# Kernel optimization log

Measured on AMD Instinct MI355X. Metric: run time of the kernel, lower is better.

## Reference

```python
import jax, jax.numpy as jnp
import numpy as np
from jax import lax

B, H, W_IN, C = 32, 32, 32, 128   # NHWC input
KH, KW = 3, 3                     # kernel size (padding 'same', stride 1)
F = 512                           # filters


def setup_inputs() -> dict:
    key = jax.random.key(0)
    ks = jax.random.split(key, 10)
    # sparse factor shapes: (KH*KW*C, 1152), (1152, F), (F, F)
    d0, d1, d2, d3 = KH * KW * C, 1152, F, F
    x = jax.random.normal(ks[0], (B, H, W_IN, C), dtype=jnp.float32)
    k0 = jax.random.normal(ks[1], (d0, d1), dtype=jnp.float32) * (1.0 / np.sqrt(d0))
    k1 = jax.random.normal(ks[2], (d1, d2), dtype=jnp.float32) * (1.0 / np.sqrt(d1))
    k2 = jax.random.normal(ks[3], (d2, d3), dtype=jnp.float32) * (1.0 / np.sqrt(d2))
    # fixed binary sparsity masks (K.constant in the original build)
    m0 = jax.random.bernoulli(ks[4], 0.1, (d0, d1)).astype(jnp.float32)
    m1 = jax.random.bernoulli(ks[5], 0.1, (d1, d2)).astype(jnp.float32)
    m2 = jax.random.bernoulli(ks[6], 0.1, (d2, d3)).astype(jnp.float32)
    scale = jax.random.normal(ks[7], (1,), dtype=jnp.float32)
    bias = jax.random.normal(ks[8], (F,), dtype=jnp.float32) * 0.01
    return {"x": x, "k0": k0, "k1": k1, "k2": k2,
            "m0": m0, "m1": m1, "m2": m2, "scale": scale, "bias": bias}


def reference(x, k0, k1, k2, m0, m1, m2, scale, bias):
    # Chained masked sparse factors collapse (associativity) to one effective
    # filter matrix of shape (KH*KW*C, F); the im2col row flatten order in the
    # original is (h, w, c), which matches an HWIO reshape exactly.
    w_eff = (k0 * m0) @ (k1 * m1) @ (k2 * m2)          # (KH*KW*C, F)
    w = (w_eff * scale[0]).reshape(KH, KW, C, F)        # fold scalar scale into kernel
    out = lax.conv_general_dilated(
        x, w, window_strides=(1, 1), padding='SAME',
        dimension_numbers=('NHWC', 'HWIO', 'NHWC'))     # (B, H, W, F)
    return out + bias
```

## Files before the change

### kernel.cpp

```cpp
#include <hip/hip_runtime.h>

typedef __attribute__((ext_vector_type(8))) short short8;
typedef __attribute__((ext_vector_type(4))) float f32x4;

typedef __attribute__((address_space(1))) const unsigned gas_u32;
typedef __attribute__((address_space(3))) unsigned las_u32;

static __device__ __forceinline__ void g2l16(const void* g, void* l) {
  __builtin_amdgcn_global_load_lds((gas_u32*)g, (las_u32*)l, 16, 0, 0);
}

static __device__ __forceinline__ short f2bf(float f) {
  union { float f; unsigned u; } v; v.f = f;
  unsigned r = (v.u + 0x7FFFu + ((v.u >> 16) & 1u)) >> 16;
  return (short)r;
}

#define MF(a_, b_, c_) __builtin_amdgcn_mfma_f32_16x16x32_bf16(a_, b_, c_, 0, 0, 0)

static __device__ __forceinline__ void xcvt_body(const float* __restrict__ x,
                                                 short* __restrict__ xbp, int i) {
  int c8 = i & 15;
  int t = i >> 4;
  int wp = t % 34, t2 = t / 34;
  int hp = t2 % 34, b = t2 / 34;
  short8 o = {};
  if (hp >= 1 && hp <= 32 && wp >= 1 && wp <= 32) {
    const f32x4* s = (const f32x4*)(x + (((size_t)((b << 5) + hp - 1) << 5) + (wp - 1)) * 128 + c8 * 8);
    f32x4 a = s[0], bb2 = s[1];
    o[0] = f2bf(a[0]); o[1] = f2bf(a[1]); o[2] = f2bf(a[2]); o[3] = f2bf(a[3]);
    o[4] = f2bf(bb2[0]); o[5] = f2bf(bb2[1]); o[6] = f2bf(bb2[2]); o[7] = f2bf(bb2[3]);
  }
  ((short8*)xbp)[i] = o;
}

__global__ __launch_bounds__(256) void k_prepw(const float* __restrict__ k0f,
                                               const float* __restrict__ m0f,
                                               const float* __restrict__ scf,
                                               const float* __restrict__ k1f,
                                               const float* __restrict__ m1f,
                                               const float* __restrict__ k2f,
                                               const float* __restrict__ m2f,
                                               short* __restrict__ w1b,
                                               short* __restrict__ w2T,
                                               short* __restrict__ w3T,
                                               const float* __restrict__ x,
                                               short* __restrict__ xbp) {
  __shared__ float tile[32][33];
  const int bb = blockIdx.x, tid = threadIdx.x;
  if (bb < 648) {
    int i = bb * 256 + tid;
    float s = scf[0];
    const f32x4* kk = (const f32x4*)k0f + (size_t)i * 2;
    const f32x4* mm = (const f32x4*)m0f + (size_t)i * 2;
    f32x4 a0 = kk[0], a1 = kk[1], b0 = mm[0], b1 = mm[1];
    short8 o;
    o[0] = f2bf(a0[0] * b0[0] * s); o[1] = f2bf(a0[1] * b0[1] * s);
    o[2] = f2bf(a0[2] * b0[2] * s); o[3] = f2bf(a0[3] * b0[3] * s);
    o[4] = f2bf(a1[0] * b1[0] * s); o[5] = f2bf(a1[1] * b1[1] * s);
    o[6] = f2bf(a1[2] * b1[2] * s); o[7] = f2bf(a1[3] * b1[3] * s);
    ((short8*)w1b)[i] = o;
  } else if (bb < 1480) {
    const float *kf, *mf; short* outp; int D, F, idx;
    if (bb < 1224) { kf = k1f; mf = m1f; outp = w2T; D = 1152; F = 512; idx = bb - 648; }
    else           { kf = k2f; mf = m2f; outp = w3T; D = 512;  F = 512; idx = bb - 1224; }
    int f0 = (idx & 15) * 32, d0 = (idx >> 4) * 32;
    int tx = tid & 31, ty = tid >> 5;
#pragma unroll
    for (int i = 0; i < 4; ++i) {
      int d = d0 + ty + i * 8;
      size_t ix = (size_t)d * F + f0 + tx;
      tile[ty + i * 8][tx] = kf[ix] * mf[ix];
    }
    __syncthreads();
#pragma unroll
    for (int i = 0; i < 4; ++i) {
      int f = f0 + ty + i * 8;
      outp[(size_t)f * D + d0 + tx] = f2bf(tile[tx][ty + i * 8]);
    }
  } else {
    xcvt_body(x, xbp, (bb - 1480) * 256 + tid);
  }
}

__global__ __launch_bounds__(256) void k_gemmx(const short* __restrict__ A,
                                               const short* __restrict__ BT,
                                               short* __restrict__ C, int M, int N, int K,
                                               const float* __restrict__ x,
                                               short* __restrict__ xbp, int xoff) {
  __shared__ __align__(16) short As[2][64][128];
  __shared__ __align__(16) short Bs[2][64][128];
  if (blockIdx.x >= 144) {
    xcvt_body(x, xbp, (xoff + (int)blockIdx.x - 144) * 256 + (int)threadIdx.x);
    return;
  }
  const int ntiles = N >> 6;
  const int m0 = (blockIdx.x / ntiles) << 6, n0 = (blockIdx.x % ntiles) << 6;
  const int tid = threadIdx.x;
  const int lane = tid & 63, wv = tid >> 6;
  const int wr = (wv >> 1) * 32, wc = (wv & 1) * 32;
  const int lr = lane & 15, lh = lane >> 4;

  const int rr = tid >> 4, sl = tid & 15;
  const int swz = sl ^ (rr & 7);
  const unsigned aOff = (unsigned)(m0 + rr) * K + swz * 8;
  const unsigned bOff = (unsigned)(n0 + rr) * K + swz * 8;
  const int ldsRow = 4 * wv;

  f32x4 acc[2][2] = {};

#define GST(buf_, kt_) do { \
    _Pragma("unroll") for (int j = 0; j < 4; ++j) \
      g2l16(A + aOff + (unsigned)j * 16u * (unsigned)K + (unsigned)(kt_) * 128u, \
            &As[buf_][j * 16 + ldsRow][0]); \
    _Pragma("unroll") for (int j = 0; j < 4; ++j) \
      g2l16(BT + bOff + (unsigned)j * 16u * (unsigned)K + (unsigned)(kt_) * 128u, \
            &Bs[buf_][j * 16 + ldsRow][0]); \
  } while (0)

  const int nk = K >> 7;
  GST(0, 0);
  asm volatile("s_waitcnt vmcnt(0)" ::: "memory");
  __builtin_amdgcn_s_barrier();

  for (int kt = 0; kt < nk; ++kt) {
    const int cur = kt & 1;
    if (kt + 1 < nk) { if (cur) GST(0, kt + 1); else GST(1, kt + 1); }
#pragma unroll
    for (int ks = 0; ks < 4; ++ks) {
      short8 af[2], bf[2];
#pragma unroll
      for (int i = 0; i < 2; ++i)
        af[i] = *(const short8*)&As[cur][wr + i * 16 + lr][((ks * 4 + lh) ^ (lr & 7)) * 8];
#pragma unroll
      for (int i = 0; i < 2; ++i)
        bf[i] = *(const short8*)&Bs[cur][wc + i * 16 + lr][((ks * 4 + lh) ^ (lr & 7)) * 8];
#pragma unroll
      for (int mi = 0; mi < 2; ++mi)
#pragma unroll
        for (int ni = 0; ni < 2; ++ni)
          acc[mi][ni] = MF(af[mi], bf[ni], acc[mi][ni]);
    }
    if (kt + 1 < nk) asm volatile("s_waitcnt vmcnt(0)" ::: "memory");
    __builtin_amdgcn_s_barrier();
  }
#pragma unroll
  for (int mi = 0; mi < 2; ++mi) {
    const int row = m0 + wr + mi * 16 + lh * 4;
#pragma unroll
    for (int ni = 0; ni < 2; ++ni) {
      const int col = n0 + wc + ni * 16 + lr;
#pragma unroll
      for (int q = 0; q < 4; ++q)
        C[(size_t)(row + q) * N + col] = f2bf(acc[mi][ni][q]);
    }
  }
#undef GST
}

#define RD_A(mf_, ks_) \
  (*(const short8*)&As[wr * 128 + (mf_) * 16 + lr][(((ks_) * 4 + lh) ^ (lr & 7)) * 8])
#define RD_B(nf_, ks_) \
  (*(const short8*)&Bs[wc * 64 + (nf_) * 16 + lr][(((ks_) * 4 + lh) ^ (lr & 7)) * 8])

#define LOADB do { \
  bfr[0][0] = RD_B(0, 0); bfr[0][1] = RD_B(0, 1); \
  bfr[1][0] = RD_B(1, 0); bfr[1][1] = RD_B(1, 1); \
  bfr[2][0] = RD_B(2, 0); bfr[2][1] = RD_B(2, 1); \
  bfr[3][0] = RD_B(3, 0); bfr[3][1] = RD_B(3, 1); } while (0)

#define STAGE_AQ(q_, tt_) do { \
  const int tc_ = (tt_) > 17 ? 17 : (tt_); \
  const int khw_ = tc_ >> 1; const int kh_ = (khw_ * 11) >> 5; const int kw_ = khw_ - kh_ * 3; \
  const int ao_ = (kh_ * 34 + kw_) * 128 + ((tc_ & 1) << 6) + (q_) * 4352; \
  g2l16(xbp + aBase + ao_, &As[(q_) * 32 + ldsA][0]); \
  g2l16(xbp + aBase + 17408 + ao_, &As[128 + (q_) * 32 + ldsA][0]); } while (0)

#define STAGE_B(tt_) do { \
  const int tc_ = (tt_) > 17 ? 17 : (tt_); \
  g2l16(wT + bBase +     tc_ * 64, &Bs[     ldsA][0]); \
  g2l16(wT + bBase + 36864 + tc_ * 64, &Bs[32 + ldsA][0]); \
  g2l16(wT + bBase + 73728 + tc_ * 64, &Bs[64 + ldsA][0]); \
  g2l16(wT + bBase + 110592 + tc_ * 64, &Bs[96 + ldsA][0]); } while (0)

#define MFMA16(p_) \
  acc[2*(p_)  ][0] = MF(a0k0, bfr[0][0], acc[2*(p_)  ][0]); \
  acc[2*(p_)  ][1] = MF(a0k0, bfr[1][0], acc[2*(p_)  ][1]); \
  acc[2*(p_)  ][2] = MF(a0k0, bfr[2][0], acc[2*(p_)  ][2]); \
  acc[2*(p_)  ][3] = MF(a0k0, bfr[3][0], acc[2*(p_)  ][3]); \
  acc[2*(p_)+1][0] = MF(a1k0, bfr[0][0], acc[2*(p_)+1][0]); \
  acc[2*(p_)+1][1] = MF(a1k0, bfr[1][0], acc[2*(p_)+1][1]); \
  acc[2*(p_)+1][2] = MF(a1k0, bfr[2][0], acc[2*(p_)+1][2]); \
  acc[2*(p_)+1][3] = MF(a1k0, bfr[3][0], acc[2*(p_)+1][3]); \
  acc[2*(p_)  ][0] = MF(a0k1, bfr[0][1], acc[2*(p_)  ][0]); \
  acc[2*(p_)  ][1] = MF(a0k1, bfr[1][1], acc[2*(p_)  ][1]); \
  acc[2*(p_)  ][2] = MF(a0k1, bfr[2][1], acc[2*(p_)  ][2]); \
  acc[2*(p_)  ][3] = MF(a0k1, bfr[3][1], acc[2*(p_)  ][3]); \
  acc[2*(p_)+1][0] = MF(a1k1, bfr[0][1], acc[2*(p_)+1][0]); \
  acc[2*(p_)+1][1] = MF(a1k1, bfr[1][1], acc[2*(p_)+1][1]); \
  acc[2*(p_)+1][2] = MF(a1k1, bfr[2][1], acc[2*(p_)+1][2]); \
  acc[2*(p_)+1][3] = MF(a1k1, bfr[3][1], acc[2*(p_)+1][3]);

#define PHASE(p_, PRE, WAITV, ...) do { \
  PRE; \
  short8 a0k0 = RD_A(2*(p_), 0),   a0k1 = RD_A(2*(p_), 1); \
  short8 a1k0 = RD_A(2*(p_)+1, 0), a1k1 = RD_A(2*(p_)+1, 1); \
  __VA_ARGS__ \
  asm volatile("s_waitcnt lgkmcnt(0)" ::: "memory"); \
  __builtin_amdgcn_sched_barrier(0); \
  __builtin_amdgcn_s_setprio(1); \
  MFMA16(p_) \
  __builtin_amdgcn_s_setprio(0); \
  WAITV; \
  __builtin_amdgcn_s_barrier(); \
} while (0)

#define VM4 asm volatile("s_waitcnt vmcnt(4)" ::: "memory")
#define VM6 asm volatile("s_waitcnt vmcnt(6)" ::: "memory")
#define VM8 asm volatile("s_waitcnt vmcnt(8)" ::: "memory")

__global__ __launch_bounds__(256, 2) void k_conv(const short* __restrict__ xbp,
                                                 const short* __restrict__ wT,
                                                 const float* __restrict__ bias,
                                                 float* __restrict__ out) {
  __shared__ __align__(16) short As[256][64];
  __shared__ __align__(16) short Bs[128][64];
  int bid = blockIdx.x;
  bid = (bid & 7) * 64 + (bid >> 3);
  const int mt = bid >> 2, nt = bid & 3;
  const int m0 = mt << 8, n0 = nt << 7;
  const int tid = threadIdx.x;
  const int lane = tid & 63, wid = tid >> 6;
  const int wr = wid >> 1, wc = wid & 1;
  const int lr = lane & 15, lh = lane >> 4;

  f32x4 acc[8][4] = {};
  short8 bfr[4][2];

  const int rsub = tid >> 3;
  const int sw = (tid & 7) ^ (rsub & 7);
  const int ldsA = wid * 8;

  const int Mb = m0 + rsub;
  const int b = Mb >> 10, h0 = (Mb >> 5) & 31, w = Mb & 31;
  const unsigned aBase = (unsigned)((b * 34 + h0) * 34 + w) * 128 + sw * 8;
  const unsigned bBase = (unsigned)(n0 + rsub) * 1152 + sw * 8;

  STAGE_B(0);
  STAGE_AQ(0, 0); STAGE_AQ(1, 0); STAGE_AQ(2, 0);
  asm volatile("s_waitcnt vmcnt(0)" ::: "memory");
  __builtin_amdgcn_s_barrier();

  for (int t = 0; t < 18; ++t) {
    const int tn = t + 1;
    PHASE(0, LOADB, VM4, STAGE_AQ(3, t););
    PHASE(1, ,      VM6, STAGE_B(tn););
    PHASE(2, ,      VM8, STAGE_AQ(0, tn); STAGE_AQ(1, tn););
    PHASE(3, ,      VM4, STAGE_AQ(2, tn););
  }
  asm volatile("s_waitcnt vmcnt(0)" ::: "memory");

  const int orow = m0 + wr * 128, ocol = n0 + wc * 64;
#pragma unroll
  for (int mf = 0; mf < 8; ++mf) {
    const int row = orow + mf * 16 + lh * 4;
#pragma unroll
    for (int nf = 0; nf < 4; ++nf) {
      const int col = ocol + nf * 16 + lr;
      const float bv = bias[col];
#pragma unroll
      for (int q = 0; q < 4; ++q)
        out[(size_t)(row + q) * 512 + col] = acc[mf][nf][q] + bv;
    }
  }
}

extern "C" void kernel_launch(void* const* d_in, const int* in_sizes, int n_in,
                              void* d_out, int out_size, void* d_ws, size_t ws_size,
                              hipStream_t stream) {
  (void)in_sizes; (void)n_in; (void)out_size; (void)ws_size;
  const float* x    = (const float*)d_in[0];
  const float* k0   = (const float*)d_in[1];
  const float* k1   = (const float*)d_in[2];
  const float* k2   = (const float*)d_in[3];
  const float* m0   = (const float*)d_in[4];
  const float* m1   = (const float*)d_in[5];
  const float* m2   = (const float*)d_in[6];
  const float* sc   = (const float*)d_in[7];
  const float* bias = (const float*)d_in[8];
  float* out = (float*)d_out;
  char* ws = (char*)d_ws;

  short* xbp = (short*)(ws);
  short* w1b = (short*)(ws + 9469952);
  short* w2T = (short*)(ws + 12124160);
  short* w3T = (short*)(ws + 13303808);
  short* A1b = (short*)(ws + 13828096);
  short* wET = (short*)(ws + 15007744);

  k_prepw<<<2248, 256, 0, stream>>>(k0, m0, sc, k1, m1, k2, m2, w1b, w2T, w3T, x, xbp);
  k_gemmx<<<916, 256, 0, stream>>>(w1b, w2T, A1b, 1152, 512, 1152, x, xbp, 768);
  k_gemmx<<<916, 256, 0, stream>>>(w3T, A1b, wET, 512, 1152, 512, x, xbp, 1540);
  k_conv<<<512, 256, 0, stream>>>(xbp, wET, bias, out);
}
```

Baseline: 69.28 us.

## Double-buffer A fragments in registers to overlap LDS reads with MFMA

Restructures the per-phase loop so the A fragments for the next phase are read from LDS into a second register set while the current phase's MFMAs run. The explicit lgkmcnt(0) wait before each MFMA block is removed, and the global-to-LDS staging order and vmcnt waits are rearranged so all four A quarters are prefetched up front. The aim is to hide LDS read latency behind matrix math. It costs extra VGPRs for the second fragment set, and correctness depends on the compiler inserting the right LDS waits, which could alter the LDS data hazards between stage and read.

New measurement: 68.94 us. About the same (-0.5%).

```diff
diff --git a/kernel.cpp b/kernel.cpp
--- a/kernel.cpp
+++ b/kernel.cpp
@@ -163,12 +163,6 @@
 #define RD_B(nf_, ks_) \
   (*(const short8*)&Bs[wc * 64 + (nf_) * 16 + lr][(((ks_) * 4 + lh) ^ (lr & 7)) * 8])
 
-#define LOADB do { \
-  bfr[0][0] = RD_B(0, 0); bfr[0][1] = RD_B(0, 1); \
-  bfr[1][0] = RD_B(1, 0); bfr[1][1] = RD_B(1, 1); \
-  bfr[2][0] = RD_B(2, 0); bfr[2][1] = RD_B(2, 1); \
-  bfr[3][0] = RD_B(3, 0); bfr[3][1] = RD_B(3, 1); } while (0)
-
 #define STAGE_AQ(q_, tt_) do { \
   const int tc_ = (tt_) > 17 ? 17 : (tt_); \
   const int khw_ = tc_ >> 1; const int kh_ = (khw_ * 11) >> 5; const int kw_ = khw_ - kh_ * 3; \
@@ -178,46 +172,33 @@
 
 #define STAGE_B(tt_) do { \
   const int tc_ = (tt_) > 17 ? 17 : (tt_); \
-  g2l16(wT + bBase +     tc_ * 64, &Bs[     ldsA][0]); \
-  g2l16(wT + bBase + 36864 + tc_ * 64, &Bs[32 + ldsA][0]); \
-  g2l16(wT + bBase + 73728 + tc_ * 64, &Bs[64 + ldsA][0]); \
+  g2l16(wT + bBase +          tc_ * 64, &Bs[     ldsA][0]); \
+  g2l16(wT + bBase +  36864 + tc_ * 64, &Bs[32 + ldsA][0]); \
+  g2l16(wT + bBase +  73728 + tc_ * 64, &Bs[64 + ldsA][0]); \
   g2l16(wT + bBase + 110592 + tc_ * 64, &Bs[96 + ldsA][0]); } while (0)
 
-#define MFMA16(p_) \
-  acc[2*(p_)  ][0] = MF(a0k0, bfr[0][0], acc[2*(p_)  ][0]); \
-  acc[2*(p_)  ][1] = MF(a0k0, bfr[1][0], acc[2*(p_)  ][1]); \
-  acc[2*(p_)  ][2] = MF(a0k0, bfr[2][0], acc[2*(p_)  ][2]); \
-  acc[2*(p_)  ][3] = MF(a0k0, bfr[3][0], acc[2*(p_)  ][3]); \
-  acc[2*(p_)+1][0] = MF(a1k0, bfr[0][0], acc[2*(p_)+1][0]); \
-  acc[2*(p_)+1][1] = MF(a1k0, bfr[1][0], acc[2*(p_)+1][1]); \
-  acc[2*(p_)+1][2] = MF(a1k0, bfr[2][0], acc[2*(p_)+1][2]); \
-  acc[2*(p_)+1][3] = MF(a1k0, bfr[3][0], acc[2*(p_)+1][3]); \
-  acc[2*(p_)  ][0] = MF(a0k1, bfr[0][1], acc[2*(p_)  ][0]); \
-  acc[2*(p_)  ][1] = MF(a0k1, bfr[1][1], acc[2*(p_)  ][1]); \
-  acc[2*(p_)  ][2] = MF(a0k1, bfr[2][1], acc[2*(p_)  ][2]); \
-  acc[2*(p_)  ][3] = MF(a0k1, bfr[3][1], acc[2*(p_)  ][3]); \
-  acc[2*(p_)+1][0] = MF(a1k1, bfr[0][1], acc[2*(p_)+1][0]); \
-  acc[2*(p_)+1][1] = MF(a1k1, bfr[1][1], acc[2*(p_)+1][1]); \
-  acc[2*(p_)+1][2] = MF(a1k1, bfr[2][1], acc[2*(p_)+1][2]); \
-  acc[2*(p_)+1][3] = MF(a1k1, bfr[3][1], acc[2*(p_)+1][3]);
-
-#define PHASE(p_, PRE, WAITV, ...) do { \
-  PRE; \
-  short8 a0k0 = RD_A(2*(p_), 0),   a0k1 = RD_A(2*(p_), 1); \
-  short8 a1k0 = RD_A(2*(p_)+1, 0), a1k1 = RD_A(2*(p_)+1, 1); \
-  __VA_ARGS__ \
-  asm volatile("s_waitcnt lgkmcnt(0)" ::: "memory"); \
-  __builtin_amdgcn_sched_barrier(0); \
-  __builtin_amdgcn_s_setprio(1); \
-  MFMA16(p_) \
-  __builtin_amdgcn_s_setprio(0); \
-  WAITV; \
-  __builtin_amdgcn_s_barrier(); \
-} while (0)
+#define MFMA_PH(p_, x0_, x1_, x2_, x3_) \
+  acc[2*(p_)  ][0] = MF(x0_, bfr[0][0], acc[2*(p_)  ][0]); \
+  acc[2*(p_)  ][1] = MF(x0_, bfr[1][0], acc[2*(p_)  ][1]); \
+  acc[2*(p_)  ][2] = MF(x0_, bfr[2][0], acc[2*(p_)  ][2]); \
+  acc[2*(p_)  ][3] = MF(x0_, bfr[3][0], acc[2*(p_)  ][3]); \
+  acc[2*(p_)+1][0] = MF(x2_, bfr[0][0], acc[2*(p_)+1][0]); \
+  acc[2*(p_)+1][1] = MF(x2_, bfr[1][0], acc[2*(p_)+1][1]); \
+  acc[2*(p_)+1][2] = MF(x2_, bfr[2][0], acc[2*(p_)+1][2]); \
+  acc[2*(p_)+1][3] = MF(x2_, bfr[3][0], acc[2*(p_)+1][3]); \
+  acc[2*(p_)  ][0] = MF(x1_, bfr[0][1], acc[2*(p_)  ][0]); \
+  acc[2*(p_)  ][1] = MF(x1_, bfr[1][1], acc[2*(p_)  ][1]); \
+  acc[2*(p_)  ][2] = MF(x1_, bfr[2][1], acc[2*(p_)  ][2]); \
+  acc[2*(p_)  ][3] = MF(x1_, bfr[3][1], acc[2*(p_)  ][3]); \
+  acc[2*(p_)+1][0] = MF(x3_, bfr[0][1], acc[2*(p_)+1][0]); \
+  acc[2*(p_)+1][1] = MF(x3_, bfr[1][1], acc[2*(p_)+1][1]); \
+  acc[2*(p_)+1][2] = MF(x3_, bfr[2][1], acc[2*(p_)+1][2]); \
+  acc[2*(p_)+1][3] = MF(x3_, bfr[3][1], acc[2*(p_)+1][3]);
 
 #define VM4 asm volatile("s_waitcnt vmcnt(4)" ::: "memory")
-#define VM6 asm volatile("s_waitcnt vmcnt(6)" ::: "memory")
 #define VM8 asm volatile("s_waitcnt vmcnt(8)" ::: "memory")
+#define SBAR __builtin_amdgcn_s_barrier()
+#define SCHED0 __builtin_amdgcn_sched_barrier(0)
 
 __global__ __launch_bounds__(256, 2) void k_conv(const short* __restrict__ xbp,
                                                  const short* __restrict__ wT,
@@ -236,6 +217,7 @@
 
   f32x4 acc[8][4] = {};
   short8 bfr[4][2];
+  short8 aA0, aA1, aA2, aA3, aB0, aB1, aB2, aB3;
 
   const int rsub = tid >> 3;
   const int sw = (tid & 7) ^ (rsub & 7);
@@ -247,16 +229,51 @@
   const unsigned bBase = (unsigned)(n0 + rsub) * 1152 + sw * 8;
 
   STAGE_B(0);
-  STAGE_AQ(0, 0); STAGE_AQ(1, 0); STAGE_AQ(2, 0);
+  STAGE_AQ(0, 0); STAGE_AQ(1, 0); STAGE_AQ(2, 0); STAGE_AQ(3, 0);
   asm volatile("s_waitcnt vmcnt(0)" ::: "memory");
-  __builtin_amdgcn_s_barrier();
+  SBAR;
+  aA0 = RD_A(0, 0); aA1 = RD_A(0, 1); aA2 = RD_A(1, 0); aA3 = RD_A(1, 1);
 
   for (int t = 0; t < 18; ++t) {
     const int tn = t + 1;
-    PHASE(0, LOADB, VM4, STAGE_AQ(3, t););
-    PHASE(1, ,      VM6, STAGE_B(tn););
-    PHASE(2, ,      VM8, STAGE_AQ(0, tn); STAGE_AQ(1, tn););
-    PHASE(3, ,      VM4, STAGE_AQ(2, tn););
+    {
+      bfr[0][0] = RD_B(0, 0); bfr[1][0] = RD_B(1, 0); bfr[2][0] = RD_B(2, 0); bfr[3][0] = RD_B(3, 0);
+      bfr[0][1] = RD_B(0, 1); bfr[1][1] = RD_B(1, 1); bfr[2][1] = RD_B(2, 1); bfr[3][1] = RD_B(3, 1);
+      aB0 = RD_A(2, 0); aB1 = RD_A(2, 1); aB2 = RD_A(3, 0); aB3 = RD_A(3, 1);
+      STAGE_AQ(0, tn);
+      SCHED0;
+      __builtin_amdgcn_s_setprio(1);
+      MFMA_PH(0, aA0, aA1, aA2, aA3)
+      __builtin_amdgcn_s_setprio(0);
+      VM4; SBAR;
+    }
+    {
+      aA0 = RD_A(4, 0); aA1 = RD_A(4, 1); aA2 = RD_A(5, 0); aA3 = RD_A(5, 1);
+      STAGE_B(tn); STAGE_AQ(1, tn);
+      SCHED0;
+      __builtin_amdgcn_s_setprio(1);
+      MFMA_PH(1, aB0, aB1, aB2, aB3)
+      __builtin_amdgcn_s_setprio(0);
+      VM8; SBAR;
+    }
+    {
+      aB0 = RD_A(6, 0); aB1 = RD_A(6, 1); aB2 = RD_A(7, 0); aB3 = RD_A(7, 1);
+      STAGE_AQ(2, tn);
+      SCHED0;
+      __builtin_amdgcn_s_setprio(1);
+      MFMA_PH(2, aA0, aA1, aA2, aA3)
+      __builtin_amdgcn_s_setprio(0);
+      VM8; SBAR;
+    }
+    {
+      aA0 = RD_A(0, 0); aA1 = RD_A(0, 1); aA2 = RD_A(1, 0); aA3 = RD_A(1, 1);
+      STAGE_AQ(3, tn);
+      SCHED0;
+      __builtin_amdgcn_s_setprio(1);
+      MFMA_PH(3, aB0, aB1, aB2, aB3)
+      __builtin_amdgcn_s_setprio(0);
+      VM4; SBAR;
+    }
   }
   asm volatile("s_waitcnt vmcnt(0)" ::: "memory");
 
```

## Load A fragments directly from global into registers, double-buffer B in LDS

Applied to the files above, without the earlier changes.

Drops the LDS staging of the activation tile (A) and has each lane load its MFMA A-fragments straight from the padded bf16 input in global memory. The weight tile (B) becomes double-buffered in LDS, with one barrier per K-step instead of four phase barriers. The aim is to free LDS, cut barrier and LDS traffic and the instruction overhead of the phased schedule. In exchange, each lane issues uncoalesced-ish 16-byte global loads whose latency sits directly before the MFMAs. A rows are duplicated across the two column waves, which doubles global/L2 reads.

New measurement: 105.9 us. 1.53x slower.

```diff
diff --git a/kernel.cpp b/kernel.cpp
--- a/kernel.cpp
+++ b/kernel.cpp
@@ -158,73 +158,21 @@
 #undef GST
 }
 
-#define RD_A(mf_, ks_) \
-  (*(const short8*)&As[wr * 128 + (mf_) * 16 + lr][(((ks_) * 4 + lh) ^ (lr & 7)) * 8])
-#define RD_B(nf_, ks_) \
-  (*(const short8*)&Bs[wc * 64 + (nf_) * 16 + lr][(((ks_) * 4 + lh) ^ (lr & 7)) * 8])
-
-#define LOADB do { \
-  bfr[0][0] = RD_B(0, 0); bfr[0][1] = RD_B(0, 1); \
-  bfr[1][0] = RD_B(1, 0); bfr[1][1] = RD_B(1, 1); \
-  bfr[2][0] = RD_B(2, 0); bfr[2][1] = RD_B(2, 1); \
-  bfr[3][0] = RD_B(3, 0); bfr[3][1] = RD_B(3, 1); } while (0)
-
-#define STAGE_AQ(q_, tt_) do { \
+#define RD_B(buf_, nf_, ks_) \
+  (*(const short8*)&Bs[buf_][wc * 64 + (nf_) * 16 + lr][(((ks_) * 4 + lh) ^ (lr & 7)) * 8])
+
+#define STAGE_B(buf_, tt_) do { \
   const int tc_ = (tt_) > 17 ? 17 : (tt_); \
-  const int khw_ = tc_ >> 1; const int kh_ = (khw_ * 11) >> 5; const int kw_ = khw_ - kh_ * 3; \
-  const int ao_ = (kh_ * 34 + kw_) * 128 + ((tc_ & 1) << 6) + (q_) * 4352; \
-  g2l16(xbp + aBase + ao_, &As[(q_) * 32 + ldsA][0]); \
-  g2l16(xbp + aBase + 17408 + ao_, &As[128 + (q_) * 32 + ldsA][0]); } while (0)
-
-#define STAGE_B(tt_) do { \
-  const int tc_ = (tt_) > 17 ? 17 : (tt_); \
-  g2l16(wT + bBase +     tc_ * 64, &Bs[     ldsA][0]); \
-  g2l16(wT + bBase + 36864 + tc_ * 64, &Bs[32 + ldsA][0]); \
-  g2l16(wT + bBase + 73728 + tc_ * 64, &Bs[64 + ldsA][0]); \
-  g2l16(wT + bBase + 110592 + tc_ * 64, &Bs[96 + ldsA][0]); } while (0)
-
-#define MFMA16(p_) \
-  acc[2*(p_)  ][0] = MF(a0k0, bfr[0][0], acc[2*(p_)  ][0]); \
-  acc[2*(p_)  ][1] = MF(a0k0, bfr[1][0], acc[2*(p_)  ][1]); \
-  acc[2*(p_)  ][2] = MF(a0k0, bfr[2][0], acc[2*(p_)  ][2]); \
-  acc[2*(p_)  ][3] = MF(a0k0, bfr[3][0], acc[2*(p_)  ][3]); \
-  acc[2*(p_)+1][0] = MF(a1k0, bfr[0][0], acc[2*(p_)+1][0]); \
-  acc[2*(p_)+1][1] = MF(a1k0, bfr[1][0], acc[2*(p_)+1][1]); \
-  acc[2*(p_)+1][2] = MF(a1k0, bfr[2][0], acc[2*(p_)+1][2]); \
-  acc[2*(p_)+1][3] = MF(a1k0, bfr[3][0], acc[2*(p_)+1][3]); \
-  acc[2*(p_)  ][0] = MF(a0k1, bfr[0][1], acc[2*(p_)  ][0]); \
-  acc[2*(p_)  ][1] = MF(a0k1, bfr[1][1], acc[2*(p_)  ][1]); \
-  acc[2*(p_)  ][2] = MF(a0k1, bfr[2][1], acc[2*(p_)  ][2]); \
-  acc[2*(p_)  ][3] = MF(a0k1, bfr[3][1], acc[2*(p_)  ][3]); \
-  acc[2*(p_)+1][0] = MF(a1k1, bfr[0][1], acc[2*(p_)+1][0]); \
-  acc[2*(p_)+1][1] = MF(a1k1, bfr[1][1], acc[2*(p_)+1][1]); \
-  acc[2*(p_)+1][2] = MF(a1k1, bfr[2][1], acc[2*(p_)+1][2]); \
-  acc[2*(p_)+1][3] = MF(a1k1, bfr[3][1], acc[2*(p_)+1][3]);
-
-#define PHASE(p_, PRE, WAITV, ...) do { \
-  PRE; \
-  short8 a0k0 = RD_A(2*(p_), 0),   a0k1 = RD_A(2*(p_), 1); \
-  short8 a1k0 = RD_A(2*(p_)+1, 0), a1k1 = RD_A(2*(p_)+1, 1); \
-  __VA_ARGS__ \
-  asm volatile("s_waitcnt lgkmcnt(0)" ::: "memory"); \
-  __builtin_amdgcn_sched_barrier(0); \
-  __builtin_amdgcn_s_setprio(1); \
-  MFMA16(p_) \
-  __builtin_amdgcn_s_setprio(0); \
-  WAITV; \
-  __builtin_amdgcn_s_barrier(); \
-} while (0)
-
-#define VM4 asm volatile("s_waitcnt vmcnt(4)" ::: "memory")
-#define VM6 asm volatile("s_waitcnt vmcnt(6)" ::: "memory")
-#define VM8 asm volatile("s_waitcnt vmcnt(8)" ::: "memory")
+  g2l16(wT + bBase +          tc_ * 64, &Bs[buf_][     ldsB][0]); \
+  g2l16(wT + bBase +  36864 + tc_ * 64, &Bs[buf_][32 + ldsB][0]); \
+  g2l16(wT + bBase +  73728 + tc_ * 64, &Bs[buf_][64 + ldsB][0]); \
+  g2l16(wT + bBase + 110592 + tc_ * 64, &Bs[buf_][96 + ldsB][0]); } while (0)
 
 __global__ __launch_bounds__(256, 2) void k_conv(const short* __restrict__ xbp,
                                                  const short* __restrict__ wT,
                                                  const float* __restrict__ bias,
                                                  float* __restrict__ out) {
-  __shared__ __align__(16) short As[256][64];
-  __shared__ __align__(16) short Bs[128][64];
+  __shared__ __align__(16) short Bs[2][128][64];
   int bid = blockIdx.x;
   bid = (bid & 7) * 64 + (bid >> 3);
   const int mt = bid >> 2, nt = bid & 3;
@@ -235,30 +183,73 @@
   const int lr = lane & 15, lh = lane >> 4;
 
   f32x4 acc[8][4] = {};
-  short8 bfr[4][2];
 
   const int rsub = tid >> 3;
   const int sw = (tid & 7) ^ (rsub & 7);
-  const int ldsA = wid * 8;
-
-  const int Mb = m0 + rsub;
-  const int b = Mb >> 10, h0 = (Mb >> 5) & 31, w = Mb & 31;
-  const unsigned aBase = (unsigned)((b * 34 + h0) * 34 + w) * 128 + sw * 8;
+  const int ldsB = wid * 8;
   const unsigned bBase = (unsigned)(n0 + rsub) * 1152 + sw * 8;
 
-  STAGE_B(0);
-  STAGE_AQ(0, 0); STAGE_AQ(1, 0); STAGE_AQ(2, 0);
+  unsigned aFB[8];
+#pragma unroll
+  for (int mf = 0; mf < 8; ++mf) {
+    const int R = m0 + wr * 128 + mf * 16 + lr;
+    const int b = R >> 10, h0 = (R >> 5) & 31, w = R & 31;
+    aFB[mf] = (unsigned)((b * 34 + h0) * 34 + w) * 128 + lh * 8;
+  }
+
+  STAGE_B(0, 0);
   asm volatile("s_waitcnt vmcnt(0)" ::: "memory");
   __builtin_amdgcn_s_barrier();
 
   for (int t = 0; t < 18; ++t) {
-    const int tn = t + 1;
-    PHASE(0, LOADB, VM4, STAGE_AQ(3, t););
-    PHASE(1, ,      VM6, STAGE_B(tn););
-    PHASE(2, ,      VM8, STAGE_AQ(0, tn); STAGE_AQ(1, tn););
-    PHASE(3, ,      VM4, STAGE_AQ(2, tn););
-  }
-  asm volatile("s_waitcnt vmcnt(0)" ::: "memory");
+    const int cur = t & 1;
+    const int khw = t >> 1;
+    const int kh = (khw * 11) >> 5, kw = khw - kh * 3;
+    const unsigned ao = (unsigned)((kh * 34 + kw) * 128 + ((t & 1) << 6));
+
+    if (cur) STAGE_B(0, t + 1); else STAGE_B(1, t + 1);
+
+    short8 bfr[4][2];
+#pragma unroll
+    for (int nf = 0; nf < 4; ++nf) {
+      bfr[nf][0] = RD_B(cur, nf, 0);
+      bfr[nf][1] = RD_B(cur, nf, 1);
+    }
+
+    {
+      short8 af[8];
+#pragma unroll
+      for (int mf = 0; mf < 8; ++mf)
+        af[mf] = *(const short8*)(xbp + aFB[mf] + ao);
+      __builtin_amdgcn_s_setprio(1);
+#pragma unroll
+      for (int mf = 0; mf < 8; ++mf) {
+        acc[mf][0] = MF(af[mf], bfr[0][0], acc[mf][0]);
+        acc[mf][1] = MF(af[mf], bfr[1][0], acc[mf][1]);
+        acc[mf][2] = MF(af[mf], bfr[2][0], acc[mf][2]);
+        acc[mf][3] = MF(af[mf], bfr[3][0], acc[mf][3]);
+      }
+      __builtin_amdgcn_s_setprio(0);
+    }
+    {
+      short8 af[8];
+#pragma unroll
+      for (int mf = 0; mf < 8; ++mf)
+        af[mf] = *(const short8*)(xbp + aFB[mf] + ao + 32);
+      __builtin_amdgcn_s_setprio(1);
+#pragma unroll
+      for (int mf = 0; mf < 8; ++mf) {
+        acc[mf][0] = MF(af[mf], bfr[0][1], acc[mf][0]);
+        acc[mf][1] = MF(af[mf], bfr[1][1], acc[mf][1]);
+        acc[mf][2] = MF(af[mf], bfr[2][1], acc[mf][2]);
+        acc[mf][3] = MF(af[mf], bfr[3][1], acc[mf][3]);
+      }
+      __builtin_amdgcn_s_setprio(0);
+    }
+
+    asm volatile("s_waitcnt vmcnt(0)" ::: "memory");
+    __builtin_amdgcn_s_barrier();
+  }
 
   const int orow = m0 + wr * 128, ocol = n0 + wc * 64;
 #pragma unroll
```

## Stage conv operands through registers instead of direct global-to-LDS loads

Applied to the files above, without the earlier changes.

Replaces the direct global_load_lds transfers for the input and weight tiles with ordinary global loads into VGPRs, followed by explicit ds_write stores into LDS. The four MFMA phases are rescheduled so each phase issues its next global loads, reads fragments, waits at a barrier, then writes the staged registers into the LDS slots that were just freed. The goal is finer control over when LDS is written and how global latency overlaps with MFMA work. The cost is more VGPRs for the staging registers, extra ds_write instructions, and an extra barrier per phase, which could hurt occupancy at two blocks per SM.

New measurement: 71.84 us. 1.04x slower.

```diff
diff --git a/kernel.cpp b/kernel.cpp
--- a/kernel.cpp
+++ b/kernel.cpp
@@ -169,19 +169,29 @@
   bfr[2][0] = RD_B(2, 0); bfr[2][1] = RD_B(2, 1); \
   bfr[3][0] = RD_B(3, 0); bfr[3][1] = RD_B(3, 1); } while (0)
 
-#define STAGE_AQ(q_, tt_) do { \
+#define LD_AQ(q_, tt_, ra_, rb_) do { \
   const int tc_ = (tt_) > 17 ? 17 : (tt_); \
   const int khw_ = tc_ >> 1; const int kh_ = (khw_ * 11) >> 5; const int kw_ = khw_ - kh_ * 3; \
   const int ao_ = (kh_ * 34 + kw_) * 128 + ((tc_ & 1) << 6) + (q_) * 4352; \
-  g2l16(xbp + aBase + ao_, &As[(q_) * 32 + ldsA][0]); \
-  g2l16(xbp + aBase + 17408 + ao_, &As[128 + (q_) * 32 + ldsA][0]); } while (0)
-
-#define STAGE_B(tt_) do { \
+  ra_ = *(const short8*)(xbp + aBase + ao_); \
+  rb_ = *(const short8*)(xbp + aBase + 17408 + ao_); } while (0)
+
+#define WR_AQ(q_, ra_, rb_) do { \
+  *(short8*)(AsF + ((q_) * 32) * 64 + dstOff) = ra_; \
+  *(short8*)(AsF + (128 + (q_) * 32) * 64 + dstOff) = rb_; } while (0)
+
+#define LD_B(tt_) do { \
   const int tc_ = (tt_) > 17 ? 17 : (tt_); \
-  g2l16(wT + bBase +     tc_ * 64, &Bs[     ldsA][0]); \
-  g2l16(wT + bBase + 36864 + tc_ * 64, &Bs[32 + ldsA][0]); \
-  g2l16(wT + bBase + 73728 + tc_ * 64, &Bs[64 + ldsA][0]); \
-  g2l16(wT + bBase + 110592 + tc_ * 64, &Bs[96 + ldsA][0]); } while (0)
+  rB0 = *(const short8*)(wT + bBase +          tc_ * 64); \
+  rB1 = *(const short8*)(wT + bBase +  36864 + tc_ * 64); \
+  rB2 = *(const short8*)(wT + bBase +  73728 + tc_ * 64); \
+  rB3 = *(const short8*)(wT + bBase + 110592 + tc_ * 64); } while (0)
+
+#define WR_B do { \
+  *(short8*)(BsF + 0 * 2048 + dstOff) = rB0; \
+  *(short8*)(BsF + 1 * 2048 + dstOff) = rB1; \
+  *(short8*)(BsF + 2 * 2048 + dstOff) = rB2; \
+  *(short8*)(BsF + 3 * 2048 + dstOff) = rB3; } while (0)
 
 #define MFMA16(p_) \
   acc[2*(p_)  ][0] = MF(a0k0, bfr[0][0], acc[2*(p_)  ][0]); \
@@ -201,23 +211,9 @@
   acc[2*(p_)+1][2] = MF(a1k1, bfr[2][1], acc[2*(p_)+1][2]); \
   acc[2*(p_)+1][3] = MF(a1k1, bfr[3][1], acc[2*(p_)+1][3]);
 
-#define PHASE(p_, PRE, WAITV, ...) do { \
-  PRE; \
-  short8 a0k0 = RD_A(2*(p_), 0),   a0k1 = RD_A(2*(p_), 1); \
-  short8 a1k0 = RD_A(2*(p_)+1, 0), a1k1 = RD_A(2*(p_)+1, 1); \
-  __VA_ARGS__ \
-  asm volatile("s_waitcnt lgkmcnt(0)" ::: "memory"); \
-  __builtin_amdgcn_sched_barrier(0); \
-  __builtin_amdgcn_s_setprio(1); \
-  MFMA16(p_) \
-  __builtin_amdgcn_s_setprio(0); \
-  WAITV; \
-  __builtin_amdgcn_s_barrier(); \
-} while (0)
-
-#define VM4 asm volatile("s_waitcnt vmcnt(4)" ::: "memory")
-#define VM6 asm volatile("s_waitcnt vmcnt(6)" ::: "memory")
-#define VM8 asm volatile("s_waitcnt vmcnt(8)" ::: "memory")
+#define SBAR __builtin_amdgcn_s_barrier()
+#define SCHED0 __builtin_amdgcn_sched_barrier(0)
+#define LGKM0 asm volatile("s_waitcnt lgkmcnt(0)" ::: "memory")
 
 __global__ __launch_bounds__(256, 2) void k_conv(const short* __restrict__ xbp,
                                                  const short* __restrict__ wT,
@@ -236,29 +232,98 @@
 
   f32x4 acc[8][4] = {};
   short8 bfr[4][2];
+  short8 rB0, rB1, rB2, rB3;
+  short8 rA0a, rA0b, rA1a, rA1b, rA2a, rA2b, rA3a, rA3b;
 
   const int rsub = tid >> 3;
   const int sw = (tid & 7) ^ (rsub & 7);
   const int ldsA = wid * 8;
+  short* AsF = &As[0][0];
+  short* BsF = &Bs[0][0];
+  const int dstOff = ldsA * 64 + lane * 8;
 
   const int Mb = m0 + rsub;
   const int b = Mb >> 10, h0 = (Mb >> 5) & 31, w = Mb & 31;
   const unsigned aBase = (unsigned)((b * 34 + h0) * 34 + w) * 128 + sw * 8;
   const unsigned bBase = (unsigned)(n0 + rsub) * 1152 + sw * 8;
 
-  STAGE_B(0);
-  STAGE_AQ(0, 0); STAGE_AQ(1, 0); STAGE_AQ(2, 0);
+  LD_B(0);
+  LD_AQ(0, 0, rA0a, rA0b); LD_AQ(1, 0, rA1a, rA1b); LD_AQ(2, 0, rA2a, rA2b);
   asm volatile("s_waitcnt vmcnt(0)" ::: "memory");
-  __builtin_amdgcn_s_barrier();
+  WR_B;
+  WR_AQ(0, rA0a, rA0b); WR_AQ(1, rA1a, rA1b); WR_AQ(2, rA2a, rA2b);
+  LD_AQ(3, 0, rA3a, rA3b);
+  LGKM0;
+  SBAR;
 
   for (int t = 0; t < 18; ++t) {
     const int tn = t + 1;
-    PHASE(0, LOADB, VM4, STAGE_AQ(3, t););
-    PHASE(1, ,      VM6, STAGE_B(tn););
-    PHASE(2, ,      VM8, STAGE_AQ(0, tn); STAGE_AQ(1, tn););
-    PHASE(3, ,      VM4, STAGE_AQ(2, tn););
-  }
-  asm volatile("s_waitcnt vmcnt(0)" ::: "memory");
+    {
+      LD_B(tn);
+      SCHED0;
+      LOADB;
+      short8 a0k0 = RD_A(0, 0), a0k1 = RD_A(0, 1);
+      short8 a1k0 = RD_A(1, 0), a1k1 = RD_A(1, 1);
+      SBAR;
+      LGKM0;
+      SCHED0;
+      asm volatile("s_waitcnt vmcnt(4)" ::: "memory");
+      WR_AQ(3, rA3a, rA3b);
+      __builtin_amdgcn_s_setprio(1);
+      MFMA16(0)
+      __builtin_amdgcn_s_setprio(0);
+      LGKM0;
+      SBAR;
+    }
+    {
+      LD_AQ(0, tn, rA0a, rA0b); LD_AQ(1, tn, rA1a, rA1b);
+      SCHED0;
+      short8 a0k0 = RD_A(2, 0), a0k1 = RD_A(2, 1);
+      short8 a1k0 = RD_A(3, 0), a1k1 = RD_A(3, 1);
+      SBAR;
+      LGKM0;
+      SCHED0;
+      asm volatile("s_waitcnt vmcnt(4)" ::: "memory");
+      WR_B;
+      __builtin_amdgcn_s_setprio(1);
+      MFMA16(1)
+      __builtin_amdgcn_s_setprio(0);
+      LGKM0;
+      SBAR;
+    }
+    {
+      LD_AQ(2, tn, rA2a, rA2b);
+      SCHED0;
+      short8 a0k0 = RD_A(4, 0), a0k1 = RD_A(4, 1);
+      short8 a1k0 = RD_A(5, 0), a1k1 = RD_A(5, 1);
+      SBAR;
+      LGKM0;
+      SCHED0;
+      asm volatile("s_waitcnt vmcnt(2)" ::: "memory");
+      WR_AQ(0, rA0a, rA0b); WR_AQ(1, rA1a, rA1b);
+      __builtin_amdgcn_s_setprio(1);
+      MFMA16(2)
+      __builtin_amdgcn_s_setprio(0);
+      LGKM0;
+      SBAR;
+    }
+    {
+      LD_AQ(3, tn, rA3a, rA3b);
+      SCHED0;
+      short8 a0k0 = RD_A(6, 0), a0k1 = RD_A(6, 1);
+      short8 a1k0 = RD_A(7, 0), a1k1 = RD_A(7, 1);
+      SBAR;
+      LGKM0;
+      SCHED0;
+      asm volatile("s_waitcnt vmcnt(2)" ::: "memory");
+      WR_AQ(2, rA2a, rA2b);
+      __builtin_amdgcn_s_setprio(1);
+      MFMA16(3)
+      __builtin_amdgcn_s_setprio(0);
+      LGKM0;
+      SBAR;
+    }
+  }
 
   const int orow = m0 + wr * 128, ocol = n0 + wc * 64;
 #pragma unroll
```
